# Performance work log

Measured on AMD Instinct MI355X. Metric: run time of the kernel, lower is better.

## Reference

```python
import jax, jax.numpy as jnp
import numpy as np

T, N = 512, 256          # timesteps, parallel envs
STATE, HID = 64, 128     # input features, GRU hidden size


def setup_inputs() -> dict:
    key = jax.random.key(0)
    k = jax.random.split(key, 6)
    inputs = jax.random.normal(k[0], (T * N, STATE), dtype=jnp.float32)
    hxs = jax.random.normal(k[1], (N, HID), dtype=jnp.float32)
    masks = (jax.random.uniform(k[2], (T * N, 1)) > 0.02).astype(jnp.float32)
    # GRU params (torch layout: gates ordered r, z, n; rows = 3*HID)
    weight_ih = jax.random.normal(k[3], (3 * HID, STATE), dtype=jnp.float32) * 0.1
    weight_hh = jax.random.normal(k[4], (3 * HID, HID), dtype=jnp.float32) * 0.1
    bias_ih = jnp.zeros((3 * HID,), dtype=jnp.float32)  # init.constant_(0)
    bias_hh = jnp.zeros((3 * HID,), dtype=jnp.float32)
    return {
        "inputs": inputs, "hxs": hxs, "masks": masks,
        "weight_ih": weight_ih, "weight_hh": weight_hh,
        "bias_ih": bias_ih, "bias_hh": bias_hh,
    }


def reference(inputs, hxs, masks, weight_ih, weight_hh, bias_ih, bias_hh):
    n, hid = hxs.shape
    t = inputs.shape[0] // n
    x = inputs.reshape(t, n, -1)       # (t, n, state)
    m = masks.reshape(t, n, 1)         # (t, n, 1)

    # Input-to-gate projections are mask-independent: precompute for all steps.
    gx = jnp.einsum('tns,gs->tng', x, weight_ih) + bias_ih  # (t, n, 3H)

    def step(h, xs):
        gx_t, m_t = xs
        h = h * m_t                                 # inline reset (fused; replaces chunk splitting)
        gh = h @ weight_hh.T + bias_hh              # (n, 3H)
        xr, xz, xn = jnp.split(gx_t, 3, axis=-1)
        hr, hz, hn = jnp.split(gh, 3, axis=-1)
        r = jax.nn.sigmoid(xr + hr)
        z = jax.nn.sigmoid(xz + hz)
        cand = jnp.tanh(xn + r * hn)
        h = (1.0 - z) * cand + z * h                # torch GRU update
        return h, h

    h_final, ys = jax.lax.scan(step, hxs, (gx, m))  # ys: (t, n, H)
    return ys.reshape(t * n, hid), h_final
```

## Files before the change

### kernel.cpp

```cpp
#include <hip/hip_runtime.h>
#include <math.h>

#define T_STEPS  512
#define N_ENVS   256
#define STATE    64
#define HID      128
#define NTHREADS 512
#define XPAD     72

typedef _Float16 half8   __attribute__((ext_vector_type(8)));
typedef _Float16 half4_t __attribute__((ext_vector_type(4)));
typedef float    floatx4 __attribute__((ext_vector_type(4)));

#define BAR() asm volatile("s_waitcnt lgkmcnt(0)\n\ts_barrier" ::: "memory")

__device__ __forceinline__ float fexp2(float v) {
    float r;
    asm("v_exp_f32 %0, %1" : "=v"(r) : "v"(v));
    return r;
}

__global__ __launch_bounds__(NTHREADS, 2) void gru_r7(
    const float* __restrict__ x,
    const float* __restrict__ h0,
    const float* __restrict__ masks,
    const float* __restrict__ wih,
    const float* __restrict__ whh,
    const float* __restrict__ bih,
    const float* __restrict__ bhh,
    float* __restrict__ out)
{
    const int b    = blockIdx.x;
    const int tid  = threadIdx.x;
    const int w    = tid >> 6;
    const int lane = tid & 63;
    const int c    = lane & 15;
    const int quad = lane >> 4;
    const int j    = 16 * w + c;

    __shared__ __align__(16) _Float16 buf[2][HID];
    __shared__ __align__(16) _Float16 xh[2][16][XPAD];
    __shared__ __align__(16) float    gxp[16][HID][4];

    const float SRZ = -1.44269504088896341f;
    const float SN  = -2.88539008177792681f;
    const float scl[3] = { SRZ, SRZ, SN };

    const int rowb[3] = { j, HID + j, 2 * HID + j };
    half8 Bh[3][4];
#pragma unroll
    for (int ti = 0; ti < 3; ++ti) {
        const int g = rowb[ti];
        const float sc = scl[ti];
#pragma unroll
        for (int kt = 0; kt < 4; ++kt) {
            const float* src = whh + (size_t)g * HID + kt * 32 + quad * 8;
            const float4 p0 = *(const float4*)(src);
            const float4 p1 = *(const float4*)(src + 4);
            half8 hb;
            hb[0] = (_Float16)(sc * p0.x); hb[1] = (_Float16)(sc * p0.y);
            hb[2] = (_Float16)(sc * p0.z); hb[3] = (_Float16)(sc * p0.w);
            hb[4] = (_Float16)(sc * p1.x); hb[5] = (_Float16)(sc * p1.y);
            hb[6] = (_Float16)(sc * p1.z); hb[7] = (_Float16)(sc * p1.w);
            Bh[ti][kt] = hb;
        }
    }
    half8 Bx[3][2];
#pragma unroll
    for (int ti = 0; ti < 3; ++ti) {
        const int g = rowb[ti];
        const float sc = scl[ti];
#pragma unroll
        for (int kt = 0; kt < 2; ++kt) {
            const float* src = wih + (size_t)g * STATE + kt * 32 + quad * 8;
            const float4 p0 = *(const float4*)(src);
            const float4 p1 = *(const float4*)(src + 4);
            half8 hb;
            hb[0] = (_Float16)(sc * p0.x); hb[1] = (_Float16)(sc * p0.y);
            hb[2] = (_Float16)(sc * p0.z); hb[3] = (_Float16)(sc * p0.w);
            hb[4] = (_Float16)(sc * p1.x); hb[5] = (_Float16)(sc * p1.y);
            hb[6] = (_Float16)(sc * p1.z); hb[7] = (_Float16)(sc * p1.w);
            Bx[ti][kt] = hb;
        }
    }

    const float br  = SRZ * (bih[j] + bhh[j]);
    const float bz  = SRZ * (bih[HID + j] + bhh[HID + j]);
    const float bxn = SN  * bih[2 * HID + j];
    const float bhn = SN  * bhh[2 * HID + j];

    float hr = h0[(size_t)b * HID + j];
    float hm = masks[b] * hr;
    if (quad == 0) buf[0][j] = (_Float16)hm;

    float4 xp = {0.f, 0.f, 0.f, 0.f};
    if (tid < 256) {
        const int k = tid >> 4, cc = (tid & 15) * 4;
        const float4 xv = *(const float4*)(x + ((size_t)k * N_ENVS + b) * STATE + cc);
        half4_t hx = {(_Float16)xv.x, (_Float16)xv.y, (_Float16)xv.z, (_Float16)xv.w};
        *(half4_t*)&xh[0][k][cc] = hx;
        xp = *(const float4*)(x + ((size_t)(16 + k) * N_ENVS + b) * STATE + cc);
    }
    float mwin     = masks[(size_t)(1  + (lane & 15)) * N_ENVS + b];
    float mwin_nxt = masks[(size_t)(17 + (lane & 15)) * N_ENVS + b];

    float o[4] = {0.f, 0.f, 0.f, 0.f};

    BAR();

    const floatx4 zero4 = {0.f, 0.f, 0.f, 0.f};

    for (int tc = 0; tc < 32; ++tc) {
        if (tc > 0) {
            const int tbp = (tc - 1) * 16;
#pragma unroll
            for (int i = 0; i < 4; ++i)
                out[((size_t)(tbp + quad * 4 + i) * N_ENVS + b) * HID + j] = o[i];
            mwin = mwin_nxt;
            const int stm = (tc + 1) * 16 + 1 + (lane & 15);
            mwin_nxt = masks[(size_t)(stm < T_STEPS ? stm : T_STEPS - 1) * N_ENVS + b];
        }
        if (tid < 256) {
            const int k = tid >> 4, cc = (tid & 15) * 4;
            half4_t hx = {(_Float16)xp.x, (_Float16)xp.y, (_Float16)xp.z, (_Float16)xp.w};
            *(half4_t*)&xh[(tc + 1) & 1][k][cc] = hx;
            const int st = (tc + 2) * 16 + k;
            if (st < T_STEPS)
                xp = *(const float4*)(x + ((size_t)st * N_ENVS + b) * STATE + cc);
        }

        {
            const _Float16* xr = &xh[tc & 1][c][0];
            half8 ax0 = *(const half8*)&xr[quad * 8];
            half8 ax1 = *(const half8*)&xr[32 + quad * 8];
            floatx4 g0 = __builtin_amdgcn_mfma_f32_16x16x32_f16(ax0, Bx[0][0], zero4, 0, 0, 0);
            floatx4 g1 = __builtin_amdgcn_mfma_f32_16x16x32_f16(ax0, Bx[1][0], zero4, 0, 0, 0);
            floatx4 g2 = __builtin_amdgcn_mfma_f32_16x16x32_f16(ax0, Bx[2][0], zero4, 0, 0, 0);
            g0 = __builtin_amdgcn_mfma_f32_16x16x32_f16(ax1, Bx[0][1], g0, 0, 0, 0);
            g1 = __builtin_amdgcn_mfma_f32_16x16x32_f16(ax1, Bx[1][1], g1, 0, 0, 0);
            g2 = __builtin_amdgcn_mfma_f32_16x16x32_f16(ax1, Bx[2][1], g2, 0, 0, 0);
#pragma unroll
            for (int i = 0; i < 4; ++i) {
                floatx4 p;
                p[0] = g0[i] + br;
                p[1] = g1[i] + bz;
                p[2] = g2[i] + bxn;
                p[3] = 0.f;
                *(floatx4*)&gxp[quad * 4 + i][j][0] = p;
            }
        }
        BAR();

#pragma unroll
        for (int s = 0; s < 16; ++s) {
            const _Float16* bufc = buf[s & 1];
            _Float16* bufn = (_Float16*)buf[(s + 1) & 1];

            half8 a0 = *(const half8*)(bufc + 0 * 32 + quad * 8);
            half8 a2 = *(const half8*)(bufc + 2 * 32 + quad * 8);
            half8 a1 = *(const half8*)(bufc + 1 * 32 + quad * 8);
            half8 a3 = *(const half8*)(bufc + 3 * 32 + quad * 8);
            const floatx4 gxh = *(const floatx4*)&gxp[s][j][0];
            const float mn = __int_as_float(__builtin_amdgcn_readlane(__float_as_int(mwin), s));

            floatx4 r_a = __builtin_amdgcn_mfma_f32_16x16x32_f16(a0, Bh[0][0], zero4, 0, 0, 0);
            floatx4 r_b = __builtin_amdgcn_mfma_f32_16x16x32_f16(a2, Bh[0][2], zero4, 0, 0, 0);
            floatx4 z_a = __builtin_amdgcn_mfma_f32_16x16x32_f16(a0, Bh[1][0], zero4, 0, 0, 0);
            floatx4 z_b = __builtin_amdgcn_mfma_f32_16x16x32_f16(a2, Bh[1][2], zero4, 0, 0, 0);
            floatx4 n_a = __builtin_amdgcn_mfma_f32_16x16x32_f16(a0, Bh[2][0], zero4, 0, 0, 0);
            floatx4 n_b = __builtin_amdgcn_mfma_f32_16x16x32_f16(a2, Bh[2][2], zero4, 0, 0, 0);
            r_a = __builtin_amdgcn_mfma_f32_16x16x32_f16(a1, Bh[0][1], r_a, 0, 0, 0);
            r_b = __builtin_amdgcn_mfma_f32_16x16x32_f16(a3, Bh[0][3], r_b, 0, 0, 0);
            z_a = __builtin_amdgcn_mfma_f32_16x16x32_f16(a1, Bh[1][1], z_a, 0, 0, 0);
            z_b = __builtin_amdgcn_mfma_f32_16x16x32_f16(a3, Bh[1][3], z_b, 0, 0, 0);
            n_a = __builtin_amdgcn_mfma_f32_16x16x32_f16(a1, Bh[2][1], n_a, 0, 0, 0);
            n_b = __builtin_amdgcn_mfma_f32_16x16x32_f16(a3, Bh[2][3], n_b, 0, 0, 0);

            const float urp = (r_a[0] + r_b[0]) + gxh[0];
            const float uzp = (z_a[0] + z_b[0]) + gxh[1];
            const float hnp = (n_a[0] + n_b[0]) + bhn;
            const float xnp = gxh[2];

            const float e_r = fexp2(urp);
            const float rg  = __builtin_amdgcn_rcpf(1.f + e_r);
            const float ap  = fmaf(rg, hnp, xnp);
            const float e_t = fexp2(-fabsf(ap));
            const float e_z = fexp2(fminf(uzp, 43.28f));
            const float opt = 1.f + e_t;
            const float num = fmaf(hm, opt, -copysignf(e_z * (1.f - e_t), ap));
            const float hnew = num * __builtin_amdgcn_rcpf(opt * (1.f + e_z));

            hm = mn * hnew;
            if (quad == 0) bufn[j] = (_Float16)hm;
            o[s & 3] = (quad == (s >> 2)) ? hnew : o[s & 3];
            hr = hnew;
            BAR();
        }
    }

    {
        const int tbp = 31 * 16;
#pragma unroll
        for (int i = 0; i < 4; ++i)
            out[((size_t)(tbp + quad * 4 + i) * N_ENVS + b) * HID + j] = o[i];
    }
    if (quad == 0)
        out[(size_t)T_STEPS * N_ENVS * HID + (size_t)b * HID + j] = hr;
}

extern "C" void kernel_launch(void* const* d_in, const int* in_sizes, int n_in,
                              void* d_out, int out_size, void* d_ws, size_t ws_size,
                              hipStream_t stream) {
    const float* x   = (const float*)d_in[0];
    const float* h0  = (const float*)d_in[1];
    const float* mk  = (const float*)d_in[2];
    const float* wih = (const float*)d_in[3];
    const float* whh = (const float*)d_in[4];
    const float* bih = (const float*)d_in[5];
    const float* bhh = (const float*)d_in[6];
    float* out = (float*)d_out;

    hipLaunchKernelGGL(gru_r7, dim3(N_ENVS), dim3(NTHREADS), 0, stream,
                       x, h0, mk, wih, whh, bih, bhh, out);
}
```

Baseline: 283.4 us.

## Redistribute input-gate projections via ds_bpermute into registers instead of LDS staging

Instead of writing the per-chunk input projections to a shared-memory array and reading them back each step after a barrier, each wave shuffles its MFMA results with ds_bpermute into per-lane register arrays for the 16 steps. This removes one block barrier per chunk and the LDS traffic. The r-gate input term and the hidden n bias are folded into the MFMA accumulator init, and the negated absolute value is folded into the exp instruction modifier. The 48 extra registers per lane raise register pressure, which could cause spills or lower occupancy.

```diff
diff --git a/kernel.cpp b/kernel.cpp
--- a/kernel.cpp
+++ b/kernel.cpp
@@ -19,8 +19,16 @@
     asm("v_exp_f32 %0, %1" : "=v"(r) : "v"(v));
     return r;
 }
-
-__global__ __launch_bounds__(NTHREADS, 2) void gru_r7(
+__device__ __forceinline__ float fexp2_nabs(float v) {
+    float r;
+    asm("v_exp_f32 %0, -|%1|" : "=v"(r) : "v"(v));
+    return r;
+}
+__device__ __forceinline__ float bpermf(int addr, float v) {
+    return __int_as_float(__builtin_amdgcn_ds_bpermute(addr, __float_as_int(v)));
+}
+
+__global__ __launch_bounds__(NTHREADS, 2) void gru_r8(
     const float* __restrict__ x,
     const float* __restrict__ h0,
     const float* __restrict__ masks,
@@ -40,7 +48,6 @@
 
     __shared__ __align__(16) _Float16 buf[2][HID];
     __shared__ __align__(16) _Float16 xh[2][16][XPAD];
-    __shared__ __align__(16) float    gxp[16][HID][4];
 
     const float SRZ = -1.44269504088896341f;
     const float SN  = -2.88539008177792681f;
@@ -89,6 +96,15 @@
     const float bxn = SN  * bih[2 * HID + j];
     const float bhn = SN  * bhh[2 * HID + j];
 
+    const floatx4 zero4 = {0.f, 0.f, 0.f, 0.f};
+    floatx4 cbhn = zero4; cbhn[0] = bhn;
+    floatx4 crin = zero4;
+
+    const int pa0 = (0 * 16 + c) * 4;
+    const int pa1 = (1 * 16 + c) * 4;
+    const int pa2 = (2 * 16 + c) * 4;
+    const int pa3 = (3 * 16 + c) * 4;
+
     float hr = h0[(size_t)b * HID + j];
     float hm = masks[b] * hr;
     if (quad == 0) buf[0][j] = (_Float16)hm;
@@ -108,8 +124,6 @@
 
     BAR();
 
-    const floatx4 zero4 = {0.f, 0.f, 0.f, 0.f};
-
     for (int tc = 0; tc < 32; ++tc) {
         if (tc > 0) {
             const int tbp = (tc - 1) * 16;
@@ -129,6 +143,7 @@
                 xp = *(const float4*)(x + ((size_t)st * N_ENVS + b) * STATE + cc);
         }
 
+        float gxr[16], gxz[16], gxn[16];
         {
             const _Float16* xr = &xh[tc & 1][c][0];
             half8 ax0 = *(const half8*)&xr[quad * 8];
@@ -141,15 +156,19 @@
             g2 = __builtin_amdgcn_mfma_f32_16x16x32_f16(ax1, Bx[2][1], g2, 0, 0, 0);
 #pragma unroll
             for (int i = 0; i < 4; ++i) {
-                floatx4 p;
-                p[0] = g0[i] + br;
-                p[1] = g1[i] + bz;
-                p[2] = g2[i] + bxn;
-                p[3] = 0.f;
-                *(floatx4*)&gxp[quad * 4 + i][j][0] = p;
+                g0[i] += br;
+                g1[i] += bz;
+                g2[i] += bxn;
             }
-        }
-        BAR();
+#pragma unroll
+            for (int s = 0; s < 16; ++s) {
+                const int a = (s >> 2) == 0 ? pa0 : (s >> 2) == 1 ? pa1
+                            : (s >> 2) == 2 ? pa2 : pa3;
+                gxr[s] = bpermf(a, g0[s & 3]);
+                gxz[s] = bpermf(a, g1[s & 3]);
+                gxn[s] = bpermf(a, g2[s & 3]);
+            }
+        }
 
 #pragma unroll
         for (int s = 0; s < 16; ++s) {
@@ -160,14 +179,15 @@
             half8 a2 = *(const half8*)(bufc + 2 * 32 + quad * 8);
             half8 a1 = *(const half8*)(bufc + 1 * 32 + quad * 8);
             half8 a3 = *(const half8*)(bufc + 3 * 32 + quad * 8);
-            const floatx4 gxh = *(const floatx4*)&gxp[s][j][0];
             const float mn = __int_as_float(__builtin_amdgcn_readlane(__float_as_int(mwin), s));
 
+            crin[0] = gxr[s];
+
             floatx4 r_a = __builtin_amdgcn_mfma_f32_16x16x32_f16(a0, Bh[0][0], zero4, 0, 0, 0);
-            floatx4 r_b = __builtin_amdgcn_mfma_f32_16x16x32_f16(a2, Bh[0][2], zero4, 0, 0, 0);
+            floatx4 r_b = __builtin_amdgcn_mfma_f32_16x16x32_f16(a2, Bh[0][2], crin,  0, 0, 0);
             floatx4 z_a = __builtin_amdgcn_mfma_f32_16x16x32_f16(a0, Bh[1][0], zero4, 0, 0, 0);
             floatx4 z_b = __builtin_amdgcn_mfma_f32_16x16x32_f16(a2, Bh[1][2], zero4, 0, 0, 0);
-            floatx4 n_a = __builtin_amdgcn_mfma_f32_16x16x32_f16(a0, Bh[2][0], zero4, 0, 0, 0);
+            floatx4 n_a = __builtin_amdgcn_mfma_f32_16x16x32_f16(a0, Bh[2][0], cbhn,  0, 0, 0);
             floatx4 n_b = __builtin_amdgcn_mfma_f32_16x16x32_f16(a2, Bh[2][2], zero4, 0, 0, 0);
             r_a = __builtin_amdgcn_mfma_f32_16x16x32_f16(a1, Bh[0][1], r_a, 0, 0, 0);
             r_b = __builtin_amdgcn_mfma_f32_16x16x32_f16(a3, Bh[0][3], r_b, 0, 0, 0);
@@ -176,15 +196,15 @@
             n_a = __builtin_amdgcn_mfma_f32_16x16x32_f16(a1, Bh[2][1], n_a, 0, 0, 0);
             n_b = __builtin_amdgcn_mfma_f32_16x16x32_f16(a3, Bh[2][3], n_b, 0, 0, 0);
 
-            const float urp = (r_a[0] + r_b[0]) + gxh[0];
-            const float uzp = (z_a[0] + z_b[0]) + gxh[1];
-            const float hnp = (n_a[0] + n_b[0]) + bhn;
-            const float xnp = gxh[2];
+            const float urp = r_a[0] + r_b[0];
+            const float uzp = (z_a[0] + z_b[0]) + gxz[s];
+            const float hnp = n_a[0] + n_b[0];
+            const float xnp = gxn[s];
 
             const float e_r = fexp2(urp);
             const float rg  = __builtin_amdgcn_rcpf(1.f + e_r);
             const float ap  = fmaf(rg, hnp, xnp);
-            const float e_t = fexp2(-fabsf(ap));
+            const float e_t = fexp2_nabs(ap);
             const float e_z = fexp2(fminf(uzp, 43.28f));
             const float opt = 1.f + e_t;
             const float num = fmaf(hm, opt, -copysignf(e_z * (1.f - e_t), ap));
@@ -193,7 +213,7 @@
             hm = mn * hnew;
             if (quad == 0) bufn[j] = (_Float16)hm;
             o[s & 3] = (quad == (s >> 2)) ? hnew : o[s & 3];
-            hr = hnew;
+            if (s == 15) hr = hnew;
             BAR();
         }
     }
@@ -220,6 +240,6 @@
     const float* bhh = (const float*)d_in[6];
     float* out = (float*)d_out;
 
-    hipLaunchKernelGGL(gru_r7, dim3(N_ENVS), dim3(NTHREADS), 0, stream,
+    hipLaunchKernelGGL(gru_r8, dim3(N_ENVS), dim3(NTHREADS), 0, stream,
                        x, h0, mk, wih, whh, bih, bhh, out);
 }
```

Measured after the change: 295.1 us. +4.1%, slower.
